# Performance work log

Measured on AMD Instinct MI355X. Metric: run time of the kernel, lower is better.

The kernel has to match this reference:

```python
import math
import jax, jax.numpy as jnp
import numpy as np

V, S, D, H, HID, L, B = 32000, 1024, 768, 12, 3072, 4, 2
HD = D // H
EPS = 1e-5
CLAMP = 1e9


def setup_inputs() -> dict:
    key = jax.random.key(0)
    ks = jax.random.split(key, 10)
    std = 0.02
    return {
        "W_emb": jax.random.normal(ks[0], (V, D), jnp.float32) * std,      # tied with lm_head
        "pos_emb": jax.random.normal(ks[1], (S, D), jnp.float32) * std,
        "norm1_g": jnp.ones((L, D), jnp.float32),
        "norm1_b": jnp.zeros((L, D), jnp.float32),
        "qkv_w": jax.random.normal(ks[2], (L, 3 * D, D), jnp.float32) * std,
        "qkv_b": jnp.zeros((L, 3 * D), jnp.float32),
        "proj_w": jax.random.normal(ks[3], (L, D, D), jnp.float32) * std,
        "proj_b": jnp.zeros((L, D), jnp.float32),
        "norm2_g": jnp.ones((L, D), jnp.float32),
        "norm2_b": jnp.zeros((L, D), jnp.float32),
        "ffn_w1": jax.random.normal(ks[4], (L, HID, D), jnp.float32) * std,
        "ffn_b1": jnp.zeros((L, HID), jnp.float32),
        "ffn_w2": jax.random.normal(ks[5], (L, D, HID), jnp.float32) * std,
        "ffn_b2": jnp.zeros((L, D), jnp.float32),
        "fin_g": jnp.ones((D,), jnp.float32),
        "fin_b": jnp.zeros((D,), jnp.float32),
        "input_ids": jax.random.randint(ks[6], (B, S), 0, V, jnp.int64),
    }


def layer_norm(x, g, b):
    mean = jnp.mean(x, axis=-1, keepdims=True)
    var = jnp.mean((x - mean) ** 2, axis=-1, keepdims=True)
    return g * ((x - mean) / jnp.sqrt(var + EPS)) + b


def attention(x, qkv_w, qkv_b, proj_w, proj_b):
    b, s, _ = x.shape
    qkv = x @ qkv_w.T + qkv_b                                  # [B,S,3D]
    qkv = qkv.reshape(b, s, H, 3 * HD).transpose(0, 2, 1, 3)   # [B,H,S,3*HD]
    q, k, v = qkv[..., :HD], qkv[..., HD:2 * HD], qkv[..., 2 * HD:]
    scaled = jnp.einsum("bhqd,bhkd->bhqk", q, k) / math.sqrt(HD)
    mask = jnp.tril(jnp.ones((s, s), bool))
    scaled = jnp.clip(jnp.where(mask, scaled, -jnp.inf), -CLAMP, CLAMP)
    attn = jax.nn.softmax(scaled, axis=-1)
    vals = jnp.einsum("bhqk,bhkd->bhqd", attn, v)
    vals = vals.transpose(0, 2, 1, 3).reshape(b, s, D)
    return vals @ proj_w.T + proj_b


def reference(W_emb, pos_emb, norm1_g, norm1_b, qkv_w, qkv_b, proj_w, proj_b,
              norm2_g, norm2_b, ffn_w1, ffn_b1, ffn_w2, ffn_b2, fin_g, fin_b,
              input_ids):
    x = W_emb[input_ids] * math.sqrt(D)          # [B,S,D]
    x = x + pos_emb[None, :x.shape[1], :]
    for i in range(L):
        h = layer_norm(x, norm1_g[i], norm1_b[i])
        x = x + attention(h, qkv_w[i], qkv_b[i], proj_w[i], proj_b[i])
        h = layer_norm(x, norm2_g[i], norm2_b[i])
        h = jax.nn.gelu(h @ ffn_w1[i].T + ffn_b1[i], approximate=False)
        x = x + h @ ffn_w2[i].T + ffn_b2[i]
    x = layer_norm(x, fin_g, fin_b)
    logits = x @ W_emb.T                         # tied lm_head, no bias
    return logits
```

## Files before the change

kernel.cpp:

```cpp
#include <hip/hip_runtime.h>
#include <hip/hip_bf16.h>
#include <math.h>

typedef __bf16 bf16_t;
typedef __bf16 bf16x8 __attribute__((ext_vector_type(8)));
typedef float f32x4 __attribute__((ext_vector_type(4)));

__device__ __forceinline__ void gload16(const bf16_t* g, bf16_t* l) {
  __builtin_amdgcn_global_load_lds(
      (const __attribute__((address_space(1))) unsigned int*)g,
      (__attribute__((address_space(3))) unsigned int*)l, 16, 0, 0);
}


template<int EPI>
__global__ __launch_bounds__(128, 3) void gemm_bt(
    const bf16_t* __restrict__ A, const bf16_t* __restrict__ W,
    const float* __restrict__ bias,
    bf16_t* __restrict__ obf, float* __restrict__ of32, bf16_t* __restrict__ vt,
    int M, int N, int K, int kLen)
{
  __shared__ bf16_t As[128 * 64];
  __shared__ bf16_t Bs[64 * 64];
  const int tid  = threadIdx.x;
  const int lane = tid & 63;
  const int w    = tid >> 6;
  const long m0 = (long)blockIdx.y * 128;
  const long n0 = (long)blockIdx.x * 64;
  const int k0 = blockIdx.z * kLen;
  const int k1 = k0 + kLen;

  f32x4 acc[4][4] = {};

  const int l7  = lane & 7;
  const int l15 = lane & 15;
  const int hi  = lane >> 4;
  const int rA  = w * 64 + l15;

  for (int kt = k0; kt < k1; kt += 64) {
#pragma unroll
    for (int i = 0; i < 8; ++i) {
      const int cl  = tid + i * 128;
      const int row = cl >> 3;
      const int j   = (cl & 7) ^ (row & 7);
      gload16(A + (m0 + row) * K + kt + (j << 3), As + cl * 8);
    }
#pragma unroll
    for (int i = 0; i < 4; ++i) {
      const int cl  = tid + i * 128;
      const int row = cl >> 3;
      const int j   = (cl & 7) ^ (row & 7);
      gload16(W + (n0 + row) * K + kt + (j << 3), Bs + cl * 8);
    }
    __syncthreads();
#pragma unroll
    for (int kk = 0; kk < 64; kk += 32) {
      const int ck = ((((kk >> 3) + hi) ^ l7) << 3);
      bf16x8 af[4], bfr[4];
#pragma unroll
      for (int m = 0; m < 4; ++m) af[m]  = *(const bf16x8*)(As + (rA + m * 16) * 64 + ck);
#pragma unroll
      for (int n = 0; n < 4; ++n) bfr[n] = *(const bf16x8*)(Bs + (l15 + n * 16) * 64 + ck);
#pragma unroll
      for (int m = 0; m < 4; ++m)
#pragma unroll
        for (int n = 0; n < 4; ++n)
          acc[m][n] = __builtin_amdgcn_mfma_f32_16x16x32_bf16(af[m], bfr[n], acc[m][n], 0, 0, 0);
    }
    __syncthreads();
  }

  const int lr = hi << 2;
#pragma unroll
  for (int n = 0; n < 4; ++n) {
    const long gcol = n0 + n * 16 + l15;
    float bv = 0.f;
    if (EPI == 0 || EPI == 1 || EPI == 5) bv = bias[gcol];
    if (EPI == 6 && k0 == 0)  bv = bias[gcol];
    const int hq = (int)gcol / 192;
    const int c  = (int)gcol - hq * 192;
#pragma unroll
    for (int m = 0; m < 4; ++m) {
      const long grow0 = m0 + w * 64 + m * 16 + lr;
#pragma unroll
      for (int r = 0; r < 4; ++r) {
        float v = acc[m][n][r] + bv;
        const long idx = (grow0 + r) * N + gcol;
        if (EPI == 0 || EPI == 5) {
          obf[idx] = (bf16_t)v;
          if (EPI == 5 && c >= 128) {
            const int row = (int)(grow0 + r);
            const int bb = row >> 10, ss = row & 1023;
            vt[(((long)bb * 12 + hq) * 64 + (c - 128)) * 1024 + ss] = (bf16_t)v;
          }
        } else if (EPI == 1) {
          v = 0.5f * v * (1.0f + erff(v * 0.70710678118654752f));
          obf[idx] = (bf16_t)v;
        } else {
          of32[(long)blockIdx.z * ((long)M * N) + idx] = v;
        }
      }
    }
  }
}

__global__ __launch_bounds__(256, 2) void gemm_logits(
    const bf16_t* __restrict__ A, const bf16_t* __restrict__ W,
    float* __restrict__ out)
{
  __shared__ bf16_t As[128 * 64];
  __shared__ bf16_t Bs[128 * 64];
  const int tid  = threadIdx.x;
  const int lane = tid & 63;
  const int w    = tid >> 6;
  const int wr   = w >> 1;
  const int wc   = w & 1;
  const int d    = blockIdx.x;
  const int wk   = (d & 7) * 500 + (d >> 3);
  const long m0  = (long)(wk & 15) * 128;
  const long n0  = (long)(wk >> 4) * 128;
  const int K = 768, N = 32000;

  f32x4 acc[4][4] = {};
  const int l7  = lane & 7;
  const int l15 = lane & 15;
  const int hi  = lane >> 4;
  const int rA  = wr * 64 + l15;
  const int rB  = wc * 64 + l15;

  for (int kt = 0; kt < K; kt += 64) {
#pragma unroll
    for (int i = 0; i < 4; ++i) {
      const int cl  = tid + i * 256;
      const int row = cl >> 3;
      const int j   = (cl & 7) ^ (row & 7);
      gload16(A + (m0 + row) * K + kt + (j << 3), As + cl * 8);
    }
#pragma unroll
    for (int i = 0; i < 4; ++i) {
      const int cl  = tid + i * 256;
      const int row = cl >> 3;
      const int j   = (cl & 7) ^ (row & 7);
      gload16(W + (n0 + row) * K + kt + (j << 3), Bs + cl * 8);
    }
    __syncthreads();
#pragma unroll
    for (int kk = 0; kk < 64; kk += 32) {
      const int ck = ((((kk >> 3) + hi) ^ l7) << 3);
      bf16x8 af[4], bfr[4];
#pragma unroll
      for (int m = 0; m < 4; ++m) af[m]  = *(const bf16x8*)(As + (rA + m * 16) * 64 + ck);
#pragma unroll
      for (int n = 0; n < 4; ++n) bfr[n] = *(const bf16x8*)(Bs + (rB + n * 16) * 64 + ck);
#pragma unroll
      for (int m = 0; m < 4; ++m)
#pragma unroll
        for (int n = 0; n < 4; ++n)
          acc[m][n] = __builtin_amdgcn_mfma_f32_16x16x32_bf16(af[m], bfr[n], acc[m][n], 0, 0, 0);
    }
    __syncthreads();
  }

  const int lr = hi << 2;
#pragma unroll
  for (int n = 0; n < 4; ++n) {
    const long gcol = n0 + wc * 64 + n * 16 + l15;
#pragma unroll
    for (int m = 0; m < 4; ++m) {
      const long grow0 = m0 + wr * 64 + m * 16 + lr;
#pragma unroll
      for (int r = 0; r < 4; ++r)
        __builtin_nontemporal_store(acc[m][n][r], &out[(grow0 + r) * N + gcol]);
    }
  }
}

__global__ __launch_bounds__(256) void attn_kernel(
    const bf16_t* __restrict__ qkv, const bf16_t* __restrict__ vT,
    bf16_t* __restrict__ aout)
{
  __shared__ bf16_t Plds[4][16 * 64];
  const int tid  = threadIdx.x;
  const int lane = tid & 63;
  const int w    = tid >> 6;
  const int wid  = blockIdx.x * 4 + w;
  const int qt   = wid & 63;
  const int bh   = wid >> 6;
  const int b    = bh / 12;
  const int h    = bh % 12;
  const int q0   = qt << 4;

  const bf16_t* base = qkv + (long)b * 1024 * 2304 + h * 192;
  const bf16_t* vtb  = vT + (long)bh * 64 * 1024;
  const int koff  = (lane >> 4) << 3;
  const int l15   = lane & 15;
  const int rbase = (lane >> 4) << 2;

  const bf16x8 qf0 = *(const bf16x8*)(base + (long)(q0 + l15) * 2304 + koff);
  const bf16x8 qf1 = *(const bf16x8*)(base + (long)(q0 + l15) * 2304 + 32 + koff);

  f32x4 acc[4] = {};
  float mrun[4], lrun[4];
#pragma unroll
  for (int r = 0; r < 4; ++r) { mrun[r] = -1e30f; lrun[r] = 0.f; }

  bf16_t* pl = &Plds[w][0];
  const int kbmax = (q0 + 15) >> 6;
  for (int kb = 0; kb <= kbmax; ++kb) {
    const int kv0 = kb << 6;
    const f32x4 z = {0.f, 0.f, 0.f, 0.f};
    f32x4 s[4];
    __builtin_amdgcn_s_setprio(1);
#pragma unroll
    for (int g = 0; g < 4; ++g) {
      const bf16_t* kr = base + 64 + (long)(kv0 + g * 16 + l15) * 2304;
      const bf16x8 ka = *(const bf16x8*)(kr + koff);
      const bf16x8 kb2 = *(const bf16x8*)(kr + 32 + koff);
      s[g] = __builtin_amdgcn_mfma_f32_16x16x32_bf16(qf0, ka, z, 0, 0, 0);
      s[g] = __builtin_amdgcn_mfma_f32_16x16x32_bf16(qf1, kb2, s[g], 0, 0, 0);
    }
    __builtin_amdgcn_s_setprio(0);

#pragma unroll
    for (int r = 0; r < 4; ++r) {
      const int qi = q0 + rbase + r;
      float v[4];
#pragma unroll
      for (int g = 0; g < 4; ++g)
        v[g] = (kv0 + g * 16 + l15 <= qi) ? s[g][r] * 0.125f : -1e9f;
      float mx = fmaxf(fmaxf(v[0], v[1]), fmaxf(v[2], v[3]));
#pragma unroll
      for (int dd = 1; dd < 16; dd <<= 1) mx = fmaxf(mx, __shfl_xor(mx, dd));
      if (mx > mrun[r] + 8.f) {
        const float sc = __expf(mrun[r] - mx);
        lrun[r] *= sc;
        acc[0][r] *= sc; acc[1][r] *= sc; acc[2][r] *= sc; acc[3][r] *= sc;
        mrun[r] = mx;
      }
      float p[4], sm = 0.f;
#pragma unroll
      for (int g = 0; g < 4; ++g) { p[g] = __expf(v[g] - mrun[r]); sm += p[g]; }
#pragma unroll
      for (int dd = 1; dd < 16; dd <<= 1) sm += __shfl_xor(sm, dd);
      lrun[r] += sm;
#pragma unroll
      for (int g = 0; g < 4; ++g)
        pl[(rbase + r) * 64 + g * 16 + l15] = (bf16_t)p[g];
    }
    asm volatile("s_waitcnt lgkmcnt(0)" ::: "memory");
    const bf16x8 pf0 = *(const bf16x8*)(pl + l15 * 64 + koff);
    const bf16x8 pf1 = *(const bf16x8*)(pl + l15 * 64 + 32 + koff);
    __builtin_amdgcn_s_setprio(1);
#pragma unroll
    for (int hh = 0; hh < 2; ++hh) {
      const bf16x8 pf = hh ? pf1 : pf0;
      const int sbase = kv0 + hh * 32 + koff;
#pragma unroll
      for (int cb = 0; cb < 4; ++cb) {
        const bf16x8 vf = *(const bf16x8*)(vtb + (long)(cb * 16 + l15) * 1024 + sbase);
        acc[cb] = __builtin_amdgcn_mfma_f32_16x16x32_bf16(pf, vf, acc[cb], 0, 0, 0);
      }
    }
    __builtin_amdgcn_s_setprio(0);
  }

#pragma unroll
  for (int cb = 0; cb < 4; ++cb)
#pragma unroll
    for (int r = 0; r < 4; ++r) {
      const float o = acc[cb][r] / lrun[r];
      aout[(long)(b * 1024 + q0 + rbase + r) * 768 + h * 64 + cb * 16 + l15] = (bf16_t)o;
    }
}

__global__ __launch_bounds__(256) void ln_kernel(
    const float* __restrict__ x, const float* __restrict__ g,
    const float* __restrict__ bta, bf16_t* __restrict__ out)
{
  const int row = blockIdx.x;
  const int tid = threadIdx.x;
  const float* xr = x + (long)row * 768;
  const float v0 = xr[tid], v1 = xr[tid + 256], v2 = xr[tid + 512];
  float s  = v0 + v1 + v2;
  float ss = v0 * v0 + v1 * v1 + v2 * v2;
#pragma unroll
  for (int d = 1; d < 64; d <<= 1) { s += __shfl_xor(s, d); ss += __shfl_xor(ss, d); }
  __shared__ float sh[8];
  const int lane = tid & 63, wv = tid >> 6;
  if (lane == 0) { sh[wv] = s; sh[4 + wv] = ss; }
  __syncthreads();
  s  = sh[0] + sh[1] + sh[2] + sh[3];
  ss = sh[4] + sh[5] + sh[6] + sh[7];
  const float mean = s * (1.0f / 768.0f);
  const float var  = ss * (1.0f / 768.0f) - mean * mean;
  const float inv  = rsqrtf(var + 1e-5f);
  bf16_t* orow = out + (long)row * 768;
  orow[tid]       = (bf16_t)(g[tid]       * ((v0 - mean) * inv) + bta[tid]);
  orow[tid + 256] = (bf16_t)(g[tid + 256] * ((v1 - mean) * inv) + bta[tid + 256]);
  orow[tid + 512] = (bf16_t)(g[tid + 512] * ((v2 - mean) * inv) + bta[tid + 512]);
}

__global__ __launch_bounds__(256) void ln_fuse2(
    float* __restrict__ x, const float* __restrict__ dl,
    const float* __restrict__ g, const float* __restrict__ bta,
    bf16_t* __restrict__ out)
{
  const int row = blockIdx.x;
  const int tid = threadIdx.x;
  float* xr = x + (long)row * 768;
  const float* d0 = dl + (long)row * 768;
  const float* d1 = dl + 1572864 + (long)row * 768;
  float v[3];
#pragma unroll
  for (int k = 0; k < 3; ++k) {
    const int c = tid + k * 256;
    const float t = xr[c] + d0[c] + d1[c];
    v[k] = t;
    xr[c] = t;
  }
  float s  = v[0] + v[1] + v[2];
  float ss = v[0] * v[0] + v[1] * v[1] + v[2] * v[2];
#pragma unroll
  for (int d = 1; d < 64; d <<= 1) { s += __shfl_xor(s, d); ss += __shfl_xor(ss, d); }
  __shared__ float sh[8];
  const int lane = tid & 63, wv = tid >> 6;
  if (lane == 0) { sh[wv] = s; sh[4 + wv] = ss; }
  __syncthreads();
  s  = sh[0] + sh[1] + sh[2] + sh[3];
  ss = sh[4] + sh[5] + sh[6] + sh[7];
  const float mean = s * (1.0f / 768.0f);
  const float var  = ss * (1.0f / 768.0f) - mean * mean;
  const float inv  = rsqrtf(var + 1e-5f);
  bf16_t* orow = out + (long)row * 768;
#pragma unroll
  for (int k = 0; k < 3; ++k) {
    const int c = tid + k * 256;
    orow[c] = (bf16_t)(g[c] * ((v[k] - mean) * inv) + bta[c]);
  }
}

__global__ __launch_bounds__(256) void embed_kernel(
    const int* __restrict__ ids, const float* __restrict__ We,
    const float* __restrict__ pos, float* __restrict__ x)
{
  const int row = blockIdx.x;
  const int tid = threadIdx.x;
  const int s = row & 1023;
  const long id = ids[row];
  const float* wr = We + id * 768;
  const float* pr = pos + (long)s * 768;
  float* xr = x + (long)row * 768;
#pragma unroll
  for (int k = 0; k < 3; ++k) {
    const int c = tid + k * 256;
    xr[c] = wr[c] * 27.712812921102035f + pr[c];
  }
}

__global__ __launch_bounds__(256) void cvt_all_kernel(
    const float* __restrict__ s0, const float* __restrict__ s1,
    const float* __restrict__ s2, const float* __restrict__ s3,
    const float* __restrict__ s4, bf16_t* __restrict__ out)
{
  const int b = blockIdx.x;
  const float* src; long rel, obase;
  if      (b < 3456)  { src = s0; rel = (long)b * 2048;          obase = 0;        }
  else if (b < 4608)  { src = s1; rel = (long)(b - 3456) * 2048; obase = 7077888;  }
  else if (b < 9216)  { src = s2; rel = (long)(b - 4608) * 2048; obase = 9437184;  }
  else if (b < 13824) { src = s3; rel = (long)(b - 9216) * 2048; obase = 18874368; }
  else                { src = s4; rel = (long)(b - 13824) * 2048; obase = 28311552; }
  const long i = rel + (long)threadIdx.x * 8;
  const f32x4 a = *(const f32x4*)(src + i);
  const f32x4 c = *(const f32x4*)(src + i + 4);
  bf16x8 o;
#pragma unroll
  for (int j = 0; j < 4; ++j) { o[j] = (bf16_t)a[j]; o[4 + j] = (bf16_t)c[j]; }
  *(bf16x8*)(out + obase + i) = o;
}

extern "C" void kernel_launch(void* const* d_in, const int* in_sizes, int n_in,
                              void* d_out, int out_size, void* d_ws, size_t ws_size,
                              hipStream_t stream)
{
  const float* W_emb = (const float*)d_in[0];
  const float* pos   = (const float*)d_in[1];
  const float* n1g   = (const float*)d_in[2];
  const float* n1b   = (const float*)d_in[3];
  const float* qkvw  = (const float*)d_in[4];
  const float* qkvb  = (const float*)d_in[5];
  const float* projw = (const float*)d_in[6];
  const float* projb = (const float*)d_in[7];
  const float* n2g   = (const float*)d_in[8];
  const float* n2b   = (const float*)d_in[9];
  const float* f1w   = (const float*)d_in[10];
  const float* f1b   = (const float*)d_in[11];
  const float* f2w   = (const float*)d_in[12];
  const float* f2b   = (const float*)d_in[13];
  const float* fing  = (const float*)d_in[14];
  const float* finb  = (const float*)d_in[15];
  const int*   ids   = (const int*)d_in[16];
  float* out = (float*)d_out;

  char* ws = (char*)d_ws;
  float*  x     = (float*)(ws);
  bf16_t* h     = (bf16_t*)(ws + 6291456);
  bf16_t* qkv   = (bf16_t*)(ws + 9437184);
  bf16_t* attn  = (bf16_t*)(ws + 18874368);
  bf16_t* ffn1o = (bf16_t*)(ws + 22020096);
  bf16_t* Wq    = (bf16_t*)(ws + 34603008);
  bf16_t* Wp    = (bf16_t*)(ws + 48758784);
  bf16_t* W1    = (bf16_t*)(ws + 53477376);
  bf16_t* W2    = (bf16_t*)(ws + 72351744);
  bf16_t* We    = (bf16_t*)(ws + 91226112);
  bf16_t* vT    = (bf16_t*)(ws + 140378112);
  float*  dpart = (float*)(ws + 143523840);

  cvt_all_kernel<<<dim3(25824), 256, 0, stream>>>(qkvw, projw, f1w, f2w, W_emb, Wq);

  embed_kernel<<<2048, 256, 0, stream>>>(ids, W_emb, pos, x);

  for (int i = 0; i < 4; ++i) {
    if (i == 0)
      ln_kernel<<<2048, 256, 0, stream>>>(x, n1g, n1b, h);
    else
      ln_fuse2<<<2048, 256, 0, stream>>>(x, dpart, n1g + i * 768, n1b + i * 768, h);
    gemm_bt<5><<<dim3(36, 16), 128, 0, stream>>>(
        h, Wq + (long)i * 2304 * 768, qkvb + i * 2304, qkv, nullptr, vT,
        2048, 2304, 768, 768);
    attn_kernel<<<384, 256, 0, stream>>>(qkv, vT, attn);
    gemm_bt<6><<<dim3(12, 16, 2), 128, 0, stream>>>(
        attn, Wp + (long)i * 768 * 768, projb + i * 768, nullptr, dpart, nullptr,
        2048, 768, 768, 384);
    ln_fuse2<<<2048, 256, 0, stream>>>(x, dpart, n2g + i * 768, n2b + i * 768, h);
    gemm_bt<1><<<dim3(48, 16), 128, 0, stream>>>(
        h, W1 + (long)i * 3072 * 768, f1b + i * 3072, ffn1o, nullptr, nullptr,
        2048, 3072, 768, 768);
    gemm_bt<6><<<dim3(12, 16, 2), 128, 0, stream>>>(
        ffn1o, W2 + (long)i * 768 * 3072, f2b + i * 768, nullptr, dpart, nullptr,
        2048, 768, 3072, 1536);
  }
  ln_fuse2<<<2048, 256, 0, stream>>>(x, dpart, fing, finb, h);
  gemm_logits<<<dim3(4000), 256, 0, stream>>>(h, We, out);
}
```

Baseline: 808.2 us.

## Widen attention query tile, fuse embed with layernorm, split-K by three

The attention kernel now has each wave handle 32 query rows instead of 16, so every K and V fragment loaded feeds two MFMA chains. Blocks drop to 2 waves, keeping the launch at 384 blocks. The embedding is fused with the first layernorm, removing one kernel and one pass over the activations. The projection and FFN2 GEMMs now split K three ways, with a layernorm that sums three partial buffers. This adds parallelism but costs extra partial-buffer traffic, and dpart must be large enough to hold the third slice.

After: 857.4 us. 6.1% more time.

```diff
diff --git a/kernel.cpp b/kernel.cpp
--- a/kernel.cpp
+++ b/kernel.cpp
@@ -175,20 +175,20 @@
   }
 }
 
-__global__ __launch_bounds__(256) void attn_kernel(
+__global__ __launch_bounds__(128) void attn_kernel(
     const bf16_t* __restrict__ qkv, const bf16_t* __restrict__ vT,
     bf16_t* __restrict__ aout)
 {
-  __shared__ bf16_t Plds[4][16 * 64];
+  __shared__ bf16_t Plds[2][32 * 64];
   const int tid  = threadIdx.x;
   const int lane = tid & 63;
   const int w    = tid >> 6;
-  const int wid  = blockIdx.x * 4 + w;
-  const int qt   = wid & 63;
-  const int bh   = wid >> 6;
+  const int wid  = blockIdx.x * 2 + w;
+  const int qt   = wid & 31;
+  const int bh   = wid >> 5;
   const int b    = bh / 12;
   const int h    = bh % 12;
-  const int q0   = qt << 4;
+  const int q0   = qt << 5;
 
   const bf16_t* base = qkv + (long)b * 1024 * 2304 + h * 192;
   const bf16_t* vtb  = vT + (long)bh * 64 * 1024;
@@ -196,69 +196,86 @@
   const int l15   = lane & 15;
   const int rbase = (lane >> 4) << 2;
 
-  const bf16x8 qf0 = *(const bf16x8*)(base + (long)(q0 + l15) * 2304 + koff);
-  const bf16x8 qf1 = *(const bf16x8*)(base + (long)(q0 + l15) * 2304 + 32 + koff);
-
-  f32x4 acc[4] = {};
-  float mrun[4], lrun[4];
-#pragma unroll
-  for (int r = 0; r < 4; ++r) { mrun[r] = -1e30f; lrun[r] = 0.f; }
+  const bf16x8 qA0 = *(const bf16x8*)(base + (long)(q0 + l15) * 2304 + koff);
+  const bf16x8 qA1 = *(const bf16x8*)(base + (long)(q0 + l15) * 2304 + 32 + koff);
+  const bf16x8 qB0 = *(const bf16x8*)(base + (long)(q0 + 16 + l15) * 2304 + koff);
+  const bf16x8 qB1 = *(const bf16x8*)(base + (long)(q0 + 16 + l15) * 2304 + 32 + koff);
+
+  f32x4 accA[4] = {}, accB[4] = {};
+  float mA[4], lA[4], mB[4], lB[4];
+#pragma unroll
+  for (int r = 0; r < 4; ++r) { mA[r] = -1e30f; lA[r] = 0.f; mB[r] = -1e30f; lB[r] = 0.f; }
 
   bf16_t* pl = &Plds[w][0];
-  const int kbmax = (q0 + 15) >> 6;
+  const int kbmax = (q0 + 31) >> 6;
   for (int kb = 0; kb <= kbmax; ++kb) {
     const int kv0 = kb << 6;
     const f32x4 z = {0.f, 0.f, 0.f, 0.f};
-    f32x4 s[4];
+    f32x4 sA[4], sB[4];
     __builtin_amdgcn_s_setprio(1);
 #pragma unroll
     for (int g = 0; g < 4; ++g) {
       const bf16_t* kr = base + 64 + (long)(kv0 + g * 16 + l15) * 2304;
-      const bf16x8 ka = *(const bf16x8*)(kr + koff);
+      const bf16x8 ka  = *(const bf16x8*)(kr + koff);
       const bf16x8 kb2 = *(const bf16x8*)(kr + 32 + koff);
-      s[g] = __builtin_amdgcn_mfma_f32_16x16x32_bf16(qf0, ka, z, 0, 0, 0);
-      s[g] = __builtin_amdgcn_mfma_f32_16x16x32_bf16(qf1, kb2, s[g], 0, 0, 0);
+      sA[g] = __builtin_amdgcn_mfma_f32_16x16x32_bf16(qA0, ka, z, 0, 0, 0);
+      sA[g] = __builtin_amdgcn_mfma_f32_16x16x32_bf16(qA1, kb2, sA[g], 0, 0, 0);
+      sB[g] = __builtin_amdgcn_mfma_f32_16x16x32_bf16(qB0, ka, z, 0, 0, 0);
+      sB[g] = __builtin_amdgcn_mfma_f32_16x16x32_bf16(qB1, kb2, sB[g], 0, 0, 0);
     }
     __builtin_amdgcn_s_setprio(0);
 
 #pragma unroll
-    for (int r = 0; r < 4; ++r) {
-      const int qi = q0 + rbase + r;
-      float v[4];
-#pragma unroll
-      for (int g = 0; g < 4; ++g)
-        v[g] = (kv0 + g * 16 + l15 <= qi) ? s[g][r] * 0.125f : -1e9f;
-      float mx = fmaxf(fmaxf(v[0], v[1]), fmaxf(v[2], v[3]));
-#pragma unroll
-      for (int dd = 1; dd < 16; dd <<= 1) mx = fmaxf(mx, __shfl_xor(mx, dd));
-      if (mx > mrun[r] + 8.f) {
-        const float sc = __expf(mrun[r] - mx);
-        lrun[r] *= sc;
-        acc[0][r] *= sc; acc[1][r] *= sc; acc[2][r] *= sc; acc[3][r] *= sc;
-        mrun[r] = mx;
+    for (int half = 0; half < 2; ++half) {
+      f32x4* s  = half ? sB : sA;
+      f32x4* ac = half ? accB : accA;
+      float* mr = half ? mB : mA;
+      float* lr = half ? lB : lA;
+      const int qbase = q0 + half * 16 + rbase;
+      const int prow  = half * 16 + rbase;
+#pragma unroll
+      for (int r = 0; r < 4; ++r) {
+        const int qi = qbase + r;
+        float v[4];
+#pragma unroll
+        for (int g = 0; g < 4; ++g)
+          v[g] = (kv0 + g * 16 + l15 <= qi) ? s[g][r] * 0.125f : -1e9f;
+        float mx = fmaxf(fmaxf(v[0], v[1]), fmaxf(v[2], v[3]));
+#pragma unroll
+        for (int dd = 1; dd < 16; dd <<= 1) mx = fmaxf(mx, __shfl_xor(mx, dd));
+        if (mx > mr[r] + 8.f) {
+          const float sc = __expf(mr[r] - mx);
+          lr[r] *= sc;
+          ac[0][r] *= sc; ac[1][r] *= sc; ac[2][r] *= sc; ac[3][r] *= sc;
+          mr[r] = mx;
+        }
+        float p[4], sm = 0.f;
+#pragma unroll
+        for (int g = 0; g < 4; ++g) { p[g] = __expf(v[g] - mr[r]); sm += p[g]; }
+#pragma unroll
+        for (int dd = 1; dd < 16; dd <<= 1) sm += __shfl_xor(sm, dd);
+        lr[r] += sm;
+#pragma unroll
+        for (int g = 0; g < 4; ++g)
+          pl[(prow + r) * 64 + g * 16 + l15] = (bf16_t)p[g];
       }
-      float p[4], sm = 0.f;
-#pragma unroll
-      for (int g = 0; g < 4; ++g) { p[g] = __expf(v[g] - mrun[r]); sm += p[g]; }
-#pragma unroll
-      for (int dd = 1; dd < 16; dd <<= 1) sm += __shfl_xor(sm, dd);
-      lrun[r] += sm;
-#pragma unroll
-      for (int g = 0; g < 4; ++g)
-        pl[(rbase + r) * 64 + g * 16 + l15] = (bf16_t)p[g];
     }
     asm volatile("s_waitcnt lgkmcnt(0)" ::: "memory");
-    const bf16x8 pf0 = *(const bf16x8*)(pl + l15 * 64 + koff);
-    const bf16x8 pf1 = *(const bf16x8*)(pl + l15 * 64 + 32 + koff);
+    const bf16x8 pA0 = *(const bf16x8*)(pl + l15 * 64 + koff);
+    const bf16x8 pA1 = *(const bf16x8*)(pl + l15 * 64 + 32 + koff);
+    const bf16x8 pB0 = *(const bf16x8*)(pl + (16 + l15) * 64 + koff);
+    const bf16x8 pB1 = *(const bf16x8*)(pl + (16 + l15) * 64 + 32 + koff);
     __builtin_amdgcn_s_setprio(1);
 #pragma unroll
     for (int hh = 0; hh < 2; ++hh) {
-      const bf16x8 pf = hh ? pf1 : pf0;
+      const bf16x8 pa = hh ? pA1 : pA0;
+      const bf16x8 pb = hh ? pB1 : pB0;
       const int sbase = kv0 + hh * 32 + koff;
 #pragma unroll
       for (int cb = 0; cb < 4; ++cb) {
         const bf16x8 vf = *(const bf16x8*)(vtb + (long)(cb * 16 + l15) * 1024 + sbase);
-        acc[cb] = __builtin_amdgcn_mfma_f32_16x16x32_bf16(pf, vf, acc[cb], 0, 0, 0);
+        accA[cb] = __builtin_amdgcn_mfma_f32_16x16x32_bf16(pa, vf, accA[cb], 0, 0, 0);
+        accB[cb] = __builtin_amdgcn_mfma_f32_16x16x32_bf16(pb, vf, accB[cb], 0, 0, 0);
       }
     }
     __builtin_amdgcn_s_setprio(0);
@@ -268,21 +285,33 @@
   for (int cb = 0; cb < 4; ++cb)
 #pragma unroll
     for (int r = 0; r < 4; ++r) {
-      const float o = acc[cb][r] / lrun[r];
-      aout[(long)(b * 1024 + q0 + rbase + r) * 768 + h * 64 + cb * 16 + l15] = (bf16_t)o;
-    }
-}
-
-__global__ __launch_bounds__(256) void ln_kernel(
-    const float* __restrict__ x, const float* __restrict__ g,
-    const float* __restrict__ bta, bf16_t* __restrict__ out)
+      const long col = h * 64 + cb * 16 + l15;
+      aout[(long)(b * 1024 + q0 + rbase + r) * 768 + col]      = (bf16_t)(accA[cb][r] / lA[r]);
+      aout[(long)(b * 1024 + q0 + 16 + rbase + r) * 768 + col] = (bf16_t)(accB[cb][r] / lB[r]);
+    }
+}
+
+__global__ __launch_bounds__(256) void ln_fuse3(
+    float* __restrict__ x, const float* __restrict__ dl,
+    const float* __restrict__ g, const float* __restrict__ bta,
+    bf16_t* __restrict__ out)
 {
   const int row = blockIdx.x;
   const int tid = threadIdx.x;
-  const float* xr = x + (long)row * 768;
-  const float v0 = xr[tid], v1 = xr[tid + 256], v2 = xr[tid + 512];
-  float s  = v0 + v1 + v2;
-  float ss = v0 * v0 + v1 * v1 + v2 * v2;
+  float* xr = x + (long)row * 768;
+  const float* d0 = dl + (long)row * 768;
+  const float* d1 = d0 + 1572864;
+  const float* d2 = d1 + 1572864;
+  float v[3];
+#pragma unroll
+  for (int k = 0; k < 3; ++k) {
+    const int c = tid + k * 256;
+    const float t = xr[c] + d0[c] + d1[c] + d2[c];
+    v[k] = t;
+    xr[c] = t;
+  }
+  float s  = v[0] + v[1] + v[2];
+  float ss = v[0] * v[0] + v[1] * v[1] + v[2] * v[2];
 #pragma unroll
   for (int d = 1; d < 64; d <<= 1) { s += __shfl_xor(s, d); ss += __shfl_xor(ss, d); }
   __shared__ float sh[8];
@@ -295,26 +324,31 @@
   const float var  = ss * (1.0f / 768.0f) - mean * mean;
   const float inv  = rsqrtf(var + 1e-5f);
   bf16_t* orow = out + (long)row * 768;
-  orow[tid]       = (bf16_t)(g[tid]       * ((v0 - mean) * inv) + bta[tid]);
-  orow[tid + 256] = (bf16_t)(g[tid + 256] * ((v1 - mean) * inv) + bta[tid + 256]);
-  orow[tid + 512] = (bf16_t)(g[tid + 512] * ((v2 - mean) * inv) + bta[tid + 512]);
-}
-
-__global__ __launch_bounds__(256) void ln_fuse2(
-    float* __restrict__ x, const float* __restrict__ dl,
-    const float* __restrict__ g, const float* __restrict__ bta,
+#pragma unroll
+  for (int k = 0; k < 3; ++k) {
+    const int c = tid + k * 256;
+    orow[c] = (bf16_t)(g[c] * ((v[k] - mean) * inv) + bta[c]);
+  }
+}
+
+__global__ __launch_bounds__(256) void embed_ln(
+    const int* __restrict__ ids, const float* __restrict__ We,
+    const float* __restrict__ pos, const float* __restrict__ g,
+    const float* __restrict__ bta, float* __restrict__ x,
     bf16_t* __restrict__ out)
 {
   const int row = blockIdx.x;
   const int tid = threadIdx.x;
+  const int sidx = row & 1023;
+  const long id = ids[row];
+  const float* wr = We + id * 768;
+  const float* pr = pos + (long)sidx * 768;
   float* xr = x + (long)row * 768;
-  const float* d0 = dl + (long)row * 768;
-  const float* d1 = dl + 1572864 + (long)row * 768;
   float v[3];
 #pragma unroll
   for (int k = 0; k < 3; ++k) {
     const int c = tid + k * 256;
-    const float t = xr[c] + d0[c] + d1[c];
+    const float t = wr[c] * 27.712812921102035f + pr[c];
     v[k] = t;
     xr[c] = t;
   }
@@ -336,24 +370,6 @@
   for (int k = 0; k < 3; ++k) {
     const int c = tid + k * 256;
     orow[c] = (bf16_t)(g[c] * ((v[k] - mean) * inv) + bta[c]);
-  }
-}
-
-__global__ __launch_bounds__(256) void embed_kernel(
-    const int* __restrict__ ids, const float* __restrict__ We,
-    const float* __restrict__ pos, float* __restrict__ x)
-{
-  const int row = blockIdx.x;
-  const int tid = threadIdx.x;
-  const int s = row & 1023;
-  const long id = ids[row];
-  const float* wr = We + id * 768;
-  const float* pr = pos + (long)s * 768;
-  float* xr = x + (long)row * 768;
-#pragma unroll
-  for (int k = 0; k < 3; ++k) {
-    const int c = tid + k * 256;
-    xr[c] = wr[c] * 27.712812921102035f + pr[c];
   }
 }
 
@@ -417,28 +433,26 @@
 
   cvt_all_kernel<<<dim3(25824), 256, 0, stream>>>(qkvw, projw, f1w, f2w, W_emb, Wq);
 
-  embed_kernel<<<2048, 256, 0, stream>>>(ids, W_emb, pos, x);
+  embed_ln<<<2048, 256, 0, stream>>>(ids, W_emb, pos, n1g, n1b, x, h);
 
   for (int i = 0; i < 4; ++i) {
-    if (i == 0)
-      ln_kernel<<<2048, 256, 0, stream>>>(x, n1g, n1b, h);
-    else
-      ln_fuse2<<<2048, 256, 0, stream>>>(x, dpart, n1g + i * 768, n1b + i * 768, h);
+    if (i > 0)
+      ln_fuse3<<<2048, 256, 0, stream>>>(x, dpart, n1g + i * 768, n1b + i * 768, h);
     gemm_bt<5><<<dim3(36, 16), 128, 0, stream>>>(
         h, Wq + (long)i * 2304 * 768, qkvb + i * 2304, qkv, nullptr, vT,
         2048, 2304, 768, 768);
-    attn_kernel<<<384, 256, 0, stream>>>(qkv, vT, attn);
-    gemm_bt<6><<<dim3(12, 16, 2), 128, 0, stream>>>(
+    attn_kernel<<<384, 128, 0, stream>>>(qkv, vT, attn);
+    gemm_bt<6><<<dim3(12, 16, 3), 128, 0, stream>>>(
         attn, Wp + (long)i * 768 * 768, projb + i * 768, nullptr, dpart, nullptr,
-        2048, 768, 768, 384);
-    ln_fuse2<<<2048, 256, 0, stream>>>(x, dpart, n2g + i * 768, n2b + i * 768, h);
+        2048, 768, 768, 256);
+    ln_fuse3<<<2048, 256, 0, stream>>>(x, dpart, n2g + i * 768, n2b + i * 768, h);
     gemm_bt<1><<<dim3(48, 16), 128, 0, stream>>>(
         h, W1 + (long)i * 3072 * 768, f1b + i * 3072, ffn1o, nullptr, nullptr,
         2048, 3072, 768, 768);
-    gemm_bt<6><<<dim3(12, 16, 2), 128, 0, stream>>>(
+    gemm_bt<6><<<dim3(12, 16, 3), 128, 0, stream>>>(
         ffn1o, W2 + (long)i * 768 * 3072, f2b + i * 768, nullptr, dpart, nullptr,
-        2048, 768, 3072, 1536);
-  }
-  ln_fuse2<<<2048, 256, 0, stream>>>(x, dpart, fing, finb, h);
+        2048, 768, 3072, 1024);
+  }
+  ln_fuse3<<<2048, 256, 0, stream>>>(x, dpart, fing, finb, h);
   gemm_logits<<<dim3(4000), 256, 0, stream>>>(h, We, out);
 }
```
